# Kernel tuning notes

Hardware: AMD Instinct MI355X
Metric: run time of the kernel (lower is better)

## Reference

```python
import jax, jax.numpy as jnp
import numpy as np

D = 512
H = 8
HD = D // H
EPS = 1e-5
NEG_INF = -1e30


def _ln(x, g, b):
    mu = jnp.mean(x, axis=-1, keepdims=True)
    var = jnp.mean(jnp.square(x - mu), axis=-1, keepdims=True)
    return (x - mu) * jax.lax.rsqrt(var + EPS) * g + b


def setup_inputs() -> dict:
    key = jax.random.key(0)
    ks = jax.random.split(key, 8)
    V, M, S = 128, 128, 514  # seq includes 2 head tokens (cls+dist)
    inp = {
        "video_embeds": jax.random.normal(ks[0], (V, D), jnp.float32),
        "music_features": jax.random.normal(ks[1], (M, S, D), jnp.float32),
        "music_masks": jnp.ones((M, S - 2), jnp.int32),
    }
    wk = jax.random.split(ks[2], 5)
    for name, k in zip(["Wq", "Wk", "Wv", "Wo", "Wl"], wk):
        inp[name] = jax.random.normal(k, (D, D), jnp.float32) * 0.02
    for name in ["bq", "bk", "bv", "bo", "bl"]:
        inp[name] = jnp.zeros((D,), jnp.float32)
    for name in ["g1", "g2", "g3"]:
        inp[name] = jnp.ones((D,), jnp.float32)
    for name in ["b1", "b2", "b3"]:
        inp[name] = jnp.zeros((D,), jnp.float32)
    return inp


def reference(video_embeds, music_features, music_masks,
              Wq, bq, Wk, bk, Wv, bv, Wo, bo, Wl, bl,
              g1, b1, g2, b2, g3, b3):
    # drop cls + dist tokens
    mf = music_features[:, 2:, :]  # (M, f, D)
    ve = _ln(video_embeds, g1, b1)  # (V, D)
    mf = _ln(mf, g1, b1)
    V = ve.shape[0]
    M, f, _ = mf.shape

    q = (ve @ Wq.T + bq).reshape(V, H, HD).transpose(1, 0, 2)        # (H, V, hd)
    k = (mf @ Wk.T + bk).reshape(M, f, H, HD).transpose(0, 2, 1, 3)  # (M, H, f, hd)
    v = (mf @ Wv.T + bv).reshape(M, f, H, HD).transpose(0, 2, 1, 3)  # (M, H, f, hd)

    logits = jnp.einsum('hvd,mhfd->vmhf', q, k) / np.sqrt(HD).astype(np.float32)
    mask = music_masks[None, :, None, :]  # (1, M, 1, f)
    logits = jnp.where(mask == 0, NEG_INF, logits)
    w = jax.nn.softmax(logits, axis=-1)
    attn = jnp.einsum('vmhf,mhfd->vmhd', w, v).reshape(V, M, D)
    attn = attn @ Wo.T + bo

    attn = _ln(attn, g2, b2)
    out = attn + (attn @ Wl.T + bl)  # dropout = identity in eval
    return _ln(out, g3, b3)
```

## Files before the change

### kernel.cpp

```cpp
#include <hip/hip_runtime.h>
#include <hip/hip_bf16.h>

typedef unsigned int uint;
typedef unsigned short ushort;
typedef __bf16 bf16;
typedef bf16 bf16x8 __attribute__((ext_vector_type(8)));
typedef float f32x4 __attribute__((ext_vector_type(4)));
typedef ushort ushort4v __attribute__((ext_vector_type(4)));

__device__ __forceinline__ float bf2f(ushort u) {
  union { uint u; float f; } v; v.u = ((uint)u) << 16; return v.f;
}
__device__ __forceinline__ ushort f2bf(float f) {
  union { float f; uint u; } v; v.f = f;
  uint u = v.u;
  uint r = (u + 0x7fffu + ((u >> 16) & 1u)) >> 16;
  return (ushort)r;
}

__device__ __forceinline__ void gl2lds16(const void* g, void* l) {
  __builtin_amdgcn_global_load_lds(
      (const __attribute__((address_space(1))) void*)g,
      (__attribute__((address_space(3))) void*)l, 16, 0, 0);
}

__device__ __forceinline__ void ln_rows0(
    int nrows, int blk, int nblk, int tid,
    const float* __restrict__ srcA,
    const float* __restrict__ g, const float* __restrict__ b,
    ushort* __restrict__ dst)
{
  const int l = tid & 63;
  const int nw = nblk * 4;
  for (int row = blk * 4 + (tid >> 6); row < nrows; row += nw) {
    const float* s = srcA + (size_t)row * 512;
    float x[8];
    float4 a0 = *(const float4*)(s + l * 4);
    float4 a1 = *(const float4*)(s + 256 + l * 4);
    x[0] = a0.x; x[1] = a0.y; x[2] = a0.z; x[3] = a0.w;
    x[4] = a1.x; x[5] = a1.y; x[6] = a1.z; x[7] = a1.w;
    float sum = 0.f, sq = 0.f;
    #pragma unroll
    for (int j = 0; j < 8; ++j) { sum += x[j]; sq += x[j] * x[j]; }
    #pragma unroll
    for (int o = 1; o < 64; o <<= 1) {
      sum += __shfl_xor(sum, o);
      sq  += __shfl_xor(sq, o);
    }
    float mu = sum * (1.f / 512.f);
    float var = sq * (1.f / 512.f) - mu * mu;
    float rstd = rsqrtf(var + 1e-5f);
    float4 g0 = *(const float4*)(g + l * 4);
    float4 g1 = *(const float4*)(g + 256 + l * 4);
    float4 b0 = *(const float4*)(b + l * 4);
    float4 b1 = *(const float4*)(b + 256 + l * 4);
    float gv[8] = {g0.x,g0.y,g0.z,g0.w,g1.x,g1.y,g1.z,g1.w};
    float bv[8] = {b0.x,b0.y,b0.z,b0.w,b1.x,b1.y,b1.z,b1.w};
    ushort* d = dst + (size_t)row * 512;
    ushort4v p0, p1;
    #pragma unroll
    for (int j = 0; j < 4; ++j) {
      p0[j] = f2bf((x[j] - mu) * rstd * gv[j] + bv[j]);
      p1[j] = f2bf((x[4+j] - mu) * rstd * gv[4+j] + bv[4+j]);
    }
    *(ushort4v*)(d + l * 4) = p0;
    *(ushort4v*)(d + 256 + l * 4) = p1;
  }
}

__device__ __forceinline__ void ln_pair(
    int mode, int wid, int tid,
    const void* __restrict__ srcA, const void* __restrict__ srcB,
    const float* __restrict__ g, const float* __restrict__ b,
    void* __restrict__ dst)
{
  const int l = tid & 63;
  const int r0 = wid * 2, r1 = r0 + 1;
  float x0[8], x1[8];
  if (mode == 1) {
    int mm0 = r0 >> 9, fi0 = r0 & 511;
    int mm1 = r1 >> 9, fi1 = r1 & 511;
    const float* s0 = (const float*)srcA + ((size_t)mm0 * 514 + 2 + fi0) * 512;
    const float* s1 = (const float*)srcA + ((size_t)mm1 * 514 + 2 + fi1) * 512;
    float4 a0 = *(const float4*)(s0 + l * 4);
    float4 a1 = *(const float4*)(s0 + 256 + l * 4);
    float4 c0 = *(const float4*)(s1 + l * 4);
    float4 c1 = *(const float4*)(s1 + 256 + l * 4);
    x0[0]=a0.x; x0[1]=a0.y; x0[2]=a0.z; x0[3]=a0.w;
    x0[4]=a1.x; x0[5]=a1.y; x0[6]=a1.z; x0[7]=a1.w;
    x1[0]=c0.x; x1[1]=c0.y; x1[2]=c0.z; x1[3]=c0.w;
    x1[4]=c1.x; x1[5]=c1.y; x1[6]=c1.z; x1[7]=c1.w;
  } else if (mode == 2) {
    const ushort* s0 = (const ushort*)srcA + (size_t)r0 * 512;
    const ushort* s1 = (const ushort*)srcA + (size_t)r1 * 512;
    uint4 u0 = *(const uint4*)(s0 + l * 8);
    uint4 u1 = *(const uint4*)(s1 + l * 8);
    x0[0]=bf2f((ushort)u0.x); x0[1]=bf2f((ushort)(u0.x>>16));
    x0[2]=bf2f((ushort)u0.y); x0[3]=bf2f((ushort)(u0.y>>16));
    x0[4]=bf2f((ushort)u0.z); x0[5]=bf2f((ushort)(u0.z>>16));
    x0[6]=bf2f((ushort)u0.w); x0[7]=bf2f((ushort)(u0.w>>16));
    x1[0]=bf2f((ushort)u1.x); x1[1]=bf2f((ushort)(u1.x>>16));
    x1[2]=bf2f((ushort)u1.y); x1[3]=bf2f((ushort)(u1.y>>16));
    x1[4]=bf2f((ushort)u1.z); x1[5]=bf2f((ushort)(u1.z>>16));
    x1[6]=bf2f((ushort)u1.w); x1[7]=bf2f((ushort)(u1.w>>16));
  } else {
    const ushort* sa0 = (const ushort*)srcA + (size_t)r0 * 512;
    const ushort* sb0 = (const ushort*)srcB + (size_t)r0 * 512;
    const ushort* sa1 = (const ushort*)srcA + (size_t)r1 * 512;
    const ushort* sb1 = (const ushort*)srcB + (size_t)r1 * 512;
    uint4 ua0 = *(const uint4*)(sa0 + l * 8);
    uint4 ub0 = *(const uint4*)(sb0 + l * 8);
    uint4 ua1 = *(const uint4*)(sa1 + l * 8);
    uint4 ub1 = *(const uint4*)(sb1 + l * 8);
    x0[0]=bf2f((ushort)ua0.x)+bf2f((ushort)ub0.x);
    x0[1]=bf2f((ushort)(ua0.x>>16))+bf2f((ushort)(ub0.x>>16));
    x0[2]=bf2f((ushort)ua0.y)+bf2f((ushort)ub0.y);
    x0[3]=bf2f((ushort)(ua0.y>>16))+bf2f((ushort)(ub0.y>>16));
    x0[4]=bf2f((ushort)ua0.z)+bf2f((ushort)ub0.z);
    x0[5]=bf2f((ushort)(ua0.z>>16))+bf2f((ushort)(ub0.z>>16));
    x0[6]=bf2f((ushort)ua0.w)+bf2f((ushort)ub0.w);
    x0[7]=bf2f((ushort)(ua0.w>>16))+bf2f((ushort)(ub0.w>>16));
    x1[0]=bf2f((ushort)ua1.x)+bf2f((ushort)ub1.x);
    x1[1]=bf2f((ushort)(ua1.x>>16))+bf2f((ushort)(ub1.x>>16));
    x1[2]=bf2f((ushort)ua1.y)+bf2f((ushort)ub1.y);
    x1[3]=bf2f((ushort)(ua1.y>>16))+bf2f((ushort)(ub1.y>>16));
    x1[4]=bf2f((ushort)ua1.z)+bf2f((ushort)ub1.z);
    x1[5]=bf2f((ushort)(ua1.z>>16))+bf2f((ushort)(ub1.z>>16));
    x1[6]=bf2f((ushort)ua1.w)+bf2f((ushort)ub1.w);
    x1[7]=bf2f((ushort)(ua1.w>>16))+bf2f((ushort)(ub1.w>>16));
  }
  float s0 = 0.f, q0 = 0.f, s1 = 0.f, q1 = 0.f;
  #pragma unroll
  for (int j = 0; j < 8; ++j) {
    s0 += x0[j]; q0 += x0[j] * x0[j];
    s1 += x1[j]; q1 += x1[j] * x1[j];
  }
  #pragma unroll
  for (int o = 1; o < 64; o <<= 1) {
    s0 += __shfl_xor(s0, o); q0 += __shfl_xor(q0, o);
    s1 += __shfl_xor(s1, o); q1 += __shfl_xor(q1, o);
  }
  float mu0 = s0 * (1.f/512.f), mu1 = s1 * (1.f/512.f);
  float rstd0 = rsqrtf(q0 * (1.f/512.f) - mu0 * mu0 + 1e-5f);
  float rstd1 = rsqrtf(q1 * (1.f/512.f) - mu1 * mu1 + 1e-5f);

  float gv[8], bv[8];
  if (mode == 1) {
    float4 g0 = *(const float4*)(g + l * 4);
    float4 g1v = *(const float4*)(g + 256 + l * 4);
    float4 b0 = *(const float4*)(b + l * 4);
    float4 b1v = *(const float4*)(b + 256 + l * 4);
    gv[0]=g0.x; gv[1]=g0.y; gv[2]=g0.z; gv[3]=g0.w;
    gv[4]=g1v.x; gv[5]=g1v.y; gv[6]=g1v.z; gv[7]=g1v.w;
    bv[0]=b0.x; bv[1]=b0.y; bv[2]=b0.z; bv[3]=b0.w;
    bv[4]=b1v.x; bv[5]=b1v.y; bv[6]=b1v.z; bv[7]=b1v.w;
  } else {
    float4 g0 = *(const float4*)(g + l * 8);
    float4 g1v = *(const float4*)(g + l * 8 + 4);
    float4 b0 = *(const float4*)(b + l * 8);
    float4 b1v = *(const float4*)(b + l * 8 + 4);
    gv[0]=g0.x; gv[1]=g0.y; gv[2]=g0.z; gv[3]=g0.w;
    gv[4]=g1v.x; gv[5]=g1v.y; gv[6]=g1v.z; gv[7]=g1v.w;
    bv[0]=b0.x; bv[1]=b0.y; bv[2]=b0.z; bv[3]=b0.w;
    bv[4]=b1v.x; bv[5]=b1v.y; bv[6]=b1v.z; bv[7]=b1v.w;
  }
  if (mode == 1) {
    ushort* d0 = (ushort*)dst + (size_t)r0 * 512;
    ushort* d1 = (ushort*)dst + (size_t)r1 * 512;
    ushort4v p00, p01, p10, p11;
    #pragma unroll
    for (int j = 0; j < 4; ++j) {
      p00[j] = f2bf((x0[j]-mu0)*rstd0*gv[j]+bv[j]);
      p01[j] = f2bf((x0[4+j]-mu0)*rstd0*gv[4+j]+bv[4+j]);
      p10[j] = f2bf((x1[j]-mu1)*rstd1*gv[j]+bv[j]);
      p11[j] = f2bf((x1[4+j]-mu1)*rstd1*gv[4+j]+bv[4+j]);
    }
    *(ushort4v*)(d0 + l * 4) = p00;
    *(ushort4v*)(d0 + 256 + l * 4) = p01;
    *(ushort4v*)(d1 + l * 4) = p10;
    *(ushort4v*)(d1 + 256 + l * 4) = p11;
  } else if (mode == 2) {
    ushort* d0 = (ushort*)dst + (size_t)r0 * 512;
    ushort* d1 = (ushort*)dst + (size_t)r1 * 512;
    uint4 o0, o1;
    o0.x = (uint)f2bf((x0[0]-mu0)*rstd0*gv[0]+bv[0]) | ((uint)f2bf((x0[1]-mu0)*rstd0*gv[1]+bv[1]) << 16);
    o0.y = (uint)f2bf((x0[2]-mu0)*rstd0*gv[2]+bv[2]) | ((uint)f2bf((x0[3]-mu0)*rstd0*gv[3]+bv[3]) << 16);
    o0.z = (uint)f2bf((x0[4]-mu0)*rstd0*gv[4]+bv[4]) | ((uint)f2bf((x0[5]-mu0)*rstd0*gv[5]+bv[5]) << 16);
    o0.w = (uint)f2bf((x0[6]-mu0)*rstd0*gv[6]+bv[6]) | ((uint)f2bf((x0[7]-mu0)*rstd0*gv[7]+bv[7]) << 16);
    o1.x = (uint)f2bf((x1[0]-mu1)*rstd1*gv[0]+bv[0]) | ((uint)f2bf((x1[1]-mu1)*rstd1*gv[1]+bv[1]) << 16);
    o1.y = (uint)f2bf((x1[2]-mu1)*rstd1*gv[2]+bv[2]) | ((uint)f2bf((x1[3]-mu1)*rstd1*gv[3]+bv[3]) << 16);
    o1.z = (uint)f2bf((x1[4]-mu1)*rstd1*gv[4]+bv[4]) | ((uint)f2bf((x1[5]-mu1)*rstd1*gv[5]+bv[5]) << 16);
    o1.w = (uint)f2bf((x1[6]-mu1)*rstd1*gv[6]+bv[6]) | ((uint)f2bf((x1[7]-mu1)*rstd1*gv[7]+bv[7]) << 16);
    *(uint4*)(d0 + l * 8) = o0;
    *(uint4*)(d1 + l * 8) = o1;
  } else {
    float* d0 = (float*)dst + (size_t)r0 * 512;
    float* d1 = (float*)dst + (size_t)r1 * 512;
    float4 a0, a1, c0, c1;
    a0.x=(x0[0]-mu0)*rstd0*gv[0]+bv[0]; a0.y=(x0[1]-mu0)*rstd0*gv[1]+bv[1];
    a0.z=(x0[2]-mu0)*rstd0*gv[2]+bv[2]; a0.w=(x0[3]-mu0)*rstd0*gv[3]+bv[3];
    a1.x=(x0[4]-mu0)*rstd0*gv[4]+bv[4]; a1.y=(x0[5]-mu0)*rstd0*gv[5]+bv[5];
    a1.z=(x0[6]-mu0)*rstd0*gv[6]+bv[6]; a1.w=(x0[7]-mu0)*rstd0*gv[7]+bv[7];
    c0.x=(x1[0]-mu1)*rstd1*gv[0]+bv[0]; c0.y=(x1[1]-mu1)*rstd1*gv[1]+bv[1];
    c0.z=(x1[2]-mu1)*rstd1*gv[2]+bv[2]; c0.w=(x1[3]-mu1)*rstd1*gv[3]+bv[3];
    c1.x=(x1[4]-mu1)*rstd1*gv[4]+bv[4]; c1.y=(x1[5]-mu1)*rstd1*gv[5]+bv[5];
    c1.z=(x1[6]-mu1)*rstd1*gv[6]+bv[6]; c1.w=(x1[7]-mu1)*rstd1*gv[7]+bv[7];
    *(float4*)(d0 + l * 8) = a0;
    *(float4*)(d0 + l * 8 + 4) = a1;
    *(float4*)(d1 + l * 8) = c0;
    *(float4*)(d1 + l * 8 + 4) = c1;
  }
}

__global__ __launch_bounds__(256) void ln512p(
    int mode, const void* __restrict__ srcA, const void* __restrict__ srcB,
    const float* __restrict__ g, const float* __restrict__ b,
    void* __restrict__ dst)
{
  ln_pair(mode, blockIdx.x * 4 + (threadIdx.x >> 6), threadIdx.x, srcA, srcB, g, b, dst);
}

struct PreArgs {
  const float* s0; const float* s1; const float* s2; const float* s3; const float* s4;
  ushort* d0; ushort* d1; ushort* d2; ushort* d3; ushort* d4;
  const float* video; const float* music;
  const float* g1; const float* b1;
  ushort* veln; ushort* mfln;
};
__global__ __launch_bounds__(256) void preamble(PreArgs a) {
  int bb = blockIdx.x;
  if (bb < 640) {
    int t = bb * 256 + threadIdx.x;
    int which = t >> 15;
    int e = (t & 32767) * 8;
    const float* s = which == 0 ? a.s0 : which == 1 ? a.s1 : which == 2 ? a.s2 : which == 3 ? a.s3 : a.s4;
    ushort*      d = which == 0 ? a.d0 : which == 1 ? a.d1 : which == 2 ? a.d2 : which == 3 ? a.d3 : a.d4;
    float4 v0 = *(const float4*)(s + e);
    float4 v1 = *(const float4*)(s + e + 4);
    uint4 o;
    o.x = (uint)f2bf(v0.x) | ((uint)f2bf(v0.y) << 16);
    o.y = (uint)f2bf(v0.z) | ((uint)f2bf(v0.w) << 16);
    o.z = (uint)f2bf(v1.x) | ((uint)f2bf(v1.y) << 16);
    o.w = (uint)f2bf(v1.z) | ((uint)f2bf(v1.w) << 16);
    *(uint4*)(d + e) = o;
  } else if (bb < 672) {
    ln_rows0(128, bb - 640, 32, threadIdx.x, a.video, a.g1, a.b1, a.veln);
  } else {
    ln_pair(1, (bb - 672) * 4 + (threadIdx.x >> 6), threadIdx.x,
            a.music, nullptr, a.g1, a.b1, a.mfln);
  }
}

__global__ __launch_bounds__(512) void gemm_kvq(
    const ushort* __restrict__ Amf, const ushort* __restrict__ Aq,
    const ushort* __restrict__ Wk, const ushort* __restrict__ Wv,
    const ushort* __restrict__ Wq,
    const float* __restrict__ bk, const float* __restrict__ bv,
    const float* __restrict__ bq,
    ushort* __restrict__ K, ushort* __restrict__ Vt, ushort* __restrict__ Q)
{
  __shared__ __align__(16) ushort As[2][256 * 64];
  __shared__ __align__(16) ushort Bks[2][128 * 64];
  __shared__ __align__(16) ushort Bvs[2][128 * 64];
  const int tid = threadIdx.x;
  const int w = tid >> 6, l = tid & 63;
  const int lg = l >> 4, lr = l & 15;
  const int wr = w >> 1, wc = w & 1;

  const bool isq = (blockIdx.y == 256);
  const int row0 = isq ? 0 : blockIdx.y * 256;
  const int col0 = blockIdx.x * 128;
  const ushort* Ap  = isq ? Aq : Amf;
  const ushort* Wkp = isq ? Wq : Wk;

  f32x4 kacc[4][4], vacc[4][4];
  #pragma unroll
  for (int i = 0; i < 4; i++)
    #pragma unroll
    for (int j = 0; j < 4; j++) {
      f32x4 z = {0.f,0.f,0.f,0.f};
      kacc[i][j] = z; vacc[i][j] = z;
    }

  size_t asrc[4], wksrc[2], wvsrc[2]; int aldst[4], wldst[2];
  {
    int r = tid >> 3, j = tid & 7;
    int koff = (j ^ (r & 7)) * 8;
    #pragma unroll
    for (int c2 = 0; c2 < 4; ++c2) {
      asrc[c2] = (size_t)(row0 + c2 * 64 + r) * 512 + koff;
      aldst[c2] = ((c2 * 64 + w * 8) * 64);
    }
    #pragma unroll
    for (int c2 = 0; c2 < 2; ++c2) {
      wksrc[c2] = (size_t)(col0 + c2 * 64 + r) * 512 + koff;
      wvsrc[c2] = wksrc[c2];
      wldst[c2] = ((c2 * 64 + w * 8) * 64);
    }
  }

  auto stage = [&](int pb, int kk) {
    #pragma unroll
    for (int c2 = 0; c2 < 4; ++c2)
      gl2lds16(Ap + asrc[c2] + kk * 64, &As[pb][aldst[c2]]);
    #pragma unroll
    for (int c2 = 0; c2 < 2; ++c2) {
      gl2lds16(Wkp + wksrc[c2] + kk * 64, &Bks[pb][wldst[c2]]);
      gl2lds16(Wv + wvsrc[c2] + kk * 64, &Bvs[pb][wldst[c2]]);
    }
  };
  auto compute = [&](int pb) {
    #pragma unroll
    for (int ks = 0; ks < 2; ++ks) {
      bf16x8 af[4], bkf[4];
      #pragma unroll
      for (int mi = 0; mi < 4; ++mi) {
        int r = wr * 64 + mi * 16 + lr;
        af[mi] = *(const bf16x8*)(&As[pb][r * 64 + ((ks * 32 + lg * 8) ^ ((r & 7) * 8))]);
      }
      #pragma unroll
      for (int ni = 0; ni < 4; ++ni) {
        int r = wc * 64 + ni * 16 + lr;
        bkf[ni] = *(const bf16x8*)(&Bks[pb][r * 64 + ((ks * 32 + lg * 8) ^ ((r & 7) * 8))]);
      }
      #pragma unroll
      for (int mi = 0; mi < 4; ++mi)
        #pragma unroll
        for (int ni = 0; ni < 4; ++ni)
          kacc[mi][ni] = __builtin_amdgcn_mfma_f32_16x16x32_bf16(af[mi], bkf[ni], kacc[mi][ni], 0, 0, 0);
      if (!isq) {
        bf16x8 bvf[4];
        #pragma unroll
        for (int ni = 0; ni < 4; ++ni) {
          int r = wc * 64 + ni * 16 + lr;
          bvf[ni] = *(const bf16x8*)(&Bvs[pb][r * 64 + ((ks * 32 + lg * 8) ^ ((r & 7) * 8))]);
        }
        #pragma unroll
        for (int mi = 0; mi < 4; ++mi)
          #pragma unroll
          for (int ni = 0; ni < 4; ++ni)
            vacc[mi][ni] = __builtin_amdgcn_mfma_f32_16x16x32_bf16(af[mi], bvf[ni], vacc[mi][ni], 0, 0, 0);
      }
    }
  };

  stage(0, 0);
  __syncthreads();
  int cur = 0;
  #pragma unroll
  for (int kk = 0; kk < 7; ++kk) {
    stage(cur ^ 1, kk + 1);
    compute(cur);
    __syncthreads();
    cur ^= 1;
  }
  compute(cur);

  #pragma unroll
  for (int ni = 0; ni < 4; ++ni) {
    int cg = col0 + wc * 64 + ni * 16 + lr;
    float bkc = isq ? bq[cg] : bk[cg];
    float bvc = isq ? 0.f : bv[cg];
    #pragma unroll
    for (int mi = 0; mi < 4; ++mi) {
      int rg0 = row0 + wr * 64 + mi * 16 + lg * 4;
      if (isq) {
        if (rg0 < 128) {
          #pragma unroll
          for (int e = 0; e < 4; ++e)
            Q[(size_t)(rg0 + e) * 512 + cg] = f2bf((kacc[mi][ni][e] + bkc) * 0.125f);
        }
      } else {
        #pragma unroll
        for (int e = 0; e < 4; ++e)
          K[(size_t)(rg0 + e) * 512 + cg] = f2bf(kacc[mi][ni][e] + bkc);
        int m = rg0 >> 9, fi = rg0 & 511;
        ushort4v pk;
        #pragma unroll
        for (int e = 0; e < 4; ++e) pk[e] = f2bf(vacc[mi][ni][e] + bvc);
        *(ushort4v*)(Vt + (size_t)(m * 512 + cg) * 512 + fi) = pk;
      }
    }
  }
}

__global__ __launch_bounds__(512) void gemm_t3w(
    const ushort* __restrict__ A, const ushort* __restrict__ W,
    const float* __restrict__ bias, ushort* __restrict__ C,
    float scale, int vt_mode)
{
  __shared__ __align__(16) ushort As[2][256 * 64];
  __shared__ __align__(16) ushort Bs[2][128 * 64];
  const int tid = threadIdx.x;
  const int w = tid >> 6, l = tid & 63;
  const int lg = l >> 4, lr = l & 15;
  const int wr = w >> 1, wc = w & 1;

  int nwg = gridDim.x * gridDim.y;
  int bid = blockIdx.y * gridDim.x + blockIdx.x;
  if ((nwg & 7) == 0) bid = (bid & 7) * (nwg >> 3) + (bid >> 3);
  const int bx = bid % gridDim.x, by = bid / gridDim.x;
  const int row0 = by * 256, col0 = bx * 128;

  f32x4 acc[4][4];
  #pragma unroll
  for (int i = 0; i < 4; i++)
    #pragma unroll
    for (int j = 0; j < 4; j++) { f32x4 z = {0.f,0.f,0.f,0.f}; acc[i][j] = z; }

  size_t asrc[4], wsrc[2]; int aldst[4], wldst[2];
  {
    int r = tid >> 3, j = tid & 7;
    int koff = (j ^ (r & 7)) * 8;
    #pragma unroll
    for (int c2 = 0; c2 < 4; ++c2) {
      asrc[c2] = (size_t)(row0 + c2 * 64 + r) * 512 + koff;
      aldst[c2] = ((c2 * 64 + (w * 8)) * 64);
    }
    #pragma unroll
    for (int c2 = 0; c2 < 2; ++c2) {
      wsrc[c2] = (size_t)(col0 + c2 * 64 + r) * 512 + koff;
      wldst[c2] = ((c2 * 64 + (w * 8)) * 64);
    }
  }

  auto stage = [&](int pb, int kk) {
    #pragma unroll
    for (int c2 = 0; c2 < 4; ++c2)
      gl2lds16(A + asrc[c2] + kk * 64, &As[pb][aldst[c2]]);
    #pragma unroll
    for (int c2 = 0; c2 < 2; ++c2)
      gl2lds16(W + wsrc[c2] + kk * 64, &Bs[pb][wldst[c2]]);
  };
  auto compute = [&](int pb) {
    #pragma unroll
    for (int ks = 0; ks < 2; ++ks) {
      bf16x8 af[4], bfr[4];
      #pragma unroll
      for (int mi = 0; mi < 4; ++mi) {
        int r = wr * 64 + mi * 16 + lr;
        af[mi] = *(const bf16x8*)(&As[pb][r * 64 + ((ks * 32 + lg * 8) ^ ((r & 7) * 8))]);
      }
      #pragma unroll
      for (int ni = 0; ni < 4; ++ni) {
        int r = wc * 64 + ni * 16 + lr;
        bfr[ni] = *(const bf16x8*)(&Bs[pb][r * 64 + ((ks * 32 + lg * 8) ^ ((r & 7) * 8))]);
      }
      #pragma unroll
      for (int mi = 0; mi < 4; ++mi)
        #pragma unroll
        for (int ni = 0; ni < 4; ++ni)
          acc[mi][ni] = __builtin_amdgcn_mfma_f32_16x16x32_bf16(af[mi], bfr[ni], acc[mi][ni], 0, 0, 0);
    }
  };

  stage(0, 0);
  __syncthreads();
  int cur = 0;
  #pragma unroll
  for (int kk = 0; kk < 7; ++kk) {
    stage(cur ^ 1, kk + 1);
    compute(cur);
    __syncthreads();
    cur ^= 1;
  }
  compute(cur);

  #pragma unroll
  for (int ni = 0; ni < 4; ++ni) {
    int cg = col0 + wc * 64 + ni * 16 + lr;
    float bc = bias[cg];
    #pragma unroll
    for (int mi = 0; mi < 4; ++mi) {
      int rg0 = row0 + wr * 64 + mi * 16 + lg * 4;
      if (!vt_mode) {
        #pragma unroll
        for (int e = 0; e < 4; ++e) {
          float v = (acc[mi][ni][e] + bc) * scale;
          C[(size_t)(rg0 + e) * 512 + cg] = f2bf(v);
        }
      } else {
        int m = rg0 >> 9, fi = rg0 & 511;
        ushort4v pk;
        #pragma unroll
        for (int e = 0; e < 4; ++e) pk[e] = f2bf((acc[mi][ni][e] + bc) * scale);
        *(ushort4v*)(C + (size_t)(m * 512 + cg) * 512 + fi) = pk;
      }
    }
  }
}

__global__ __launch_bounds__(256) void attn_kernel(
    const ushort* __restrict__ q, const ushort* __restrict__ k,
    const ushort* __restrict__ vt, const int* __restrict__ masks,
    ushort* __restrict__ attn)
{
  __shared__ __align__(16) ushort Qs[128 * 64];
  __shared__ __align__(16) ushort Ks[2][64 * 64];
  __shared__ __align__(16) ushort Vs[2][64 * 64];
  __shared__ __align__(16) ushort Ps[4][32 * 64];
  __shared__ float maskf[2][64];
  __shared__ float stats[4][32];

  const int tid = threadIdx.x;
  const int w = tid >> 6, l = tid & 63;
  const int lg = l >> 4, lr = l & 15;
  const int m = blockIdx.x >> 3, h = blockIdx.x & 7;

  const size_t kbase = (size_t)(m * 512) * 512 + h * 64;
  const size_t vbase = (size_t)(m * 512 + h * 64) * 512;

  int sr = tid >> 2;
  auto stageKV = [&](int pb, int it) {
    const int f0 = it * 64;
    #pragma unroll
    for (int c2 = 0; c2 < 2; ++c2) {
      int c = c2 * 256 + tid;
      int r = c >> 3, j = c & 7;
      int off = (j * 8) ^ ((r & 7) * 8);
      gl2lds16(k + kbase + (size_t)(f0 + r) * 512 + off, &Ks[pb][(c2 * 256 + w * 64) * 8]);
      gl2lds16(vt + vbase + (size_t)r * 512 + f0 + off, &Vs[pb][(c2 * 256 + w * 64) * 8]);
    }
    if (tid < 64) maskf[pb][tid] = masks[m * 512 + f0 + tid] ? 0.f : -1e30f;
  };

  #pragma unroll
  for (int c2 = 0; c2 < 4; ++c2) {
    int c = c2 * 256 + tid;
    int r = c >> 3, j = c & 7;
    gl2lds16(q + (size_t)r * 512 + h * 64 + ((j * 8) ^ ((r & 7) * 8)),
             Qs + (c2 * 256 + w * 64) * 8);
  }
  stageKV(0, 0);
  __syncthreads();

  f32x4 acc[2][4];
  #pragma unroll
  for (int i = 0; i < 2; i++)
    #pragma unroll
    for (int j = 0; j < 4; j++) { f32x4 z = {0.f,0.f,0.f,0.f}; acc[i][j] = z; }
  float m_run[2] = {-INFINITY, -INFINITY};
  float l_run[2] = {0.f, 0.f};
  bf16x8 qf[2][2];
  #pragma unroll
  for (int nv = 0; nv < 2; ++nv)
    #pragma unroll
    for (int k2 = 0; k2 < 2; ++k2) {
      int v = w * 32 + nv * 16 + lr;
      qf[nv][k2] = *(const bf16x8*)(Qs + v * 64 + ((k2 * 32 + lg * 8) ^ ((v & 7) * 8)));
    }

  int cur = 0;
  for (int it = 0; it < 8; ++it) {
    if (it < 7) stageKV(cur ^ 1, it + 1);

    f32x4 s[4][2];
    #pragma unroll
    for (int mi = 0; mi < 4; mi++)
      #pragma unroll
      for (int nv = 0; nv < 2; nv++) { f32x4 z = {0.f,0.f,0.f,0.f}; s[mi][nv] = z; }
    #pragma unroll
    for (int k2 = 0; k2 < 2; ++k2) {
      bf16x8 kf[4];
      #pragma unroll
      for (int mi = 0; mi < 4; ++mi) {
        int f = mi * 16 + lr;
        kf[mi] = *(const bf16x8*)(&Ks[cur][f * 64 + ((k2 * 32 + lg * 8) ^ ((f & 7) * 8))]);
      }
      __builtin_amdgcn_s_setprio(1);
      #pragma unroll
      for (int mi = 0; mi < 4; ++mi)
        #pragma unroll
        for (int nv = 0; nv < 2; ++nv)
          s[mi][nv] = __builtin_amdgcn_mfma_f32_16x16x32_bf16(kf[mi], qf[nv][k2], s[mi][nv], 0, 0, 0);
      __builtin_amdgcn_s_setprio(0);
    }

    float mk[4][4];
    #pragma unroll
    for (int mi = 0; mi < 4; mi++)
      #pragma unroll
      for (int e = 0; e < 4; e++) mk[mi][e] = maskf[cur][mi * 16 + lg * 4 + e];

    #pragma unroll
    for (int nv = 0; nv < 2; ++nv) {
      float pmax = -INFINITY;
      #pragma unroll
      for (int mi = 0; mi < 4; mi++)
        #pragma unroll
        for (int e = 0; e < 4; e++) {
          s[mi][nv][e] += mk[mi][e];
          pmax = fmaxf(pmax, s[mi][nv][e]);
        }
      pmax = fmaxf(pmax, __shfl_xor(pmax, 16));
      pmax = fmaxf(pmax, __shfl_xor(pmax, 32));
      bool skip = __all(pmax - m_run[nv] <= 8.f);
      float mnew = skip ? m_run[nv] : fmaxf(m_run[nv], pmax);
      float sc = skip ? 1.f : __expf(m_run[nv] - mnew);
      float csum = 0.f;
      int vloc = nv * 16 + lr;
      #pragma unroll
      for (int mi = 0; mi < 4; mi++) {
        ushort4v pk;
        #pragma unroll
        for (int e = 0; e < 4; e++) {
          float p = __expf(s[mi][nv][e] - mnew);
          csum += p;
          pk[e] = f2bf(p);
        }
        int f = mi * 16 + lg * 4;
        *(ushort4v*)(&Ps[w][vloc * 64 + (f ^ ((vloc & 7) * 8))]) = pk;
      }
      csum += __shfl_xor(csum, 16);
      csum += __shfl_xor(csum, 32);
      l_run[nv] = l_run[nv] * sc + csum;
      m_run[nv] = mnew;
      if (lg == 0) stats[w][vloc] = sc;
      if (!skip) {
        int mi2 = nv;
        #pragma unroll
        for (int e = 0; e < 4; ++e) {
          float scv = stats[w][mi2 * 16 + lg * 4 + e];
          #pragma unroll
          for (int nd = 0; nd < 4; ++nd) acc[mi2][nd][e] *= scv;
        }
      }
    }

    #pragma unroll
    for (int k2 = 0; k2 < 2; ++k2) {
      bf16x8 pf[2], vf[4];
      #pragma unroll
      for (int mi2 = 0; mi2 < 2; ++mi2) {
        int vloc = mi2 * 16 + lr;
        pf[mi2] = *(const bf16x8*)(&Ps[w][vloc * 64 + ((k2 * 32 + lg * 8) ^ ((vloc & 7) * 8))]);
      }
      #pragma unroll
      for (int nd = 0; nd < 4; ++nd) {
        int d = nd * 16 + lr;
        vf[nd] = *(const bf16x8*)(&Vs[cur][d * 64 + ((k2 * 32 + lg * 8) ^ ((d & 7) * 8))]);
      }
      __builtin_amdgcn_s_setprio(1);
      #pragma unroll
      for (int mi2 = 0; mi2 < 2; ++mi2)
        #pragma unroll
        for (int nd = 0; nd < 4; ++nd)
          acc[mi2][nd] = __builtin_amdgcn_mfma_f32_16x16x32_bf16(pf[mi2], vf[nd], acc[mi2][nd], 0, 0, 0);
      __builtin_amdgcn_s_setprio(0);
    }
    __syncthreads();
    cur ^= 1;
  }

  #pragma unroll
  for (int nv = 0; nv < 2; ++nv)
    if (lg == 0) stats[w][nv * 16 + lr] = 1.f / l_run[nv];
  #pragma unroll
  for (int mi2 = 0; mi2 < 2; ++mi2)
    #pragma unroll
    for (int e = 0; e < 4; ++e) {
      float invl = stats[w][mi2 * 16 + lg * 4 + e];
      int vg = w * 32 + mi2 * 16 + lg * 4 + e;
      #pragma unroll
      for (int nd = 0; nd < 4; ++nd) {
        int d = nd * 16 + lr;
        attn[(size_t)(vg * 128 + m) * 512 + h * 64 + d] = f2bf(acc[mi2][nd][e] * invl);
      }
    }
}

extern "C" void kernel_launch(void* const* d_in, const int* in_sizes, int n_in,
                              void* d_out, int out_size, void* d_ws, size_t ws_size,
                              hipStream_t stream) {
  const float* video = (const float*)d_in[0];
  const float* music = (const float*)d_in[1];
  const int*   masks = (const int*)d_in[2];
  const float* Wq = (const float*)d_in[3];
  const float* Wk = (const float*)d_in[4];
  const float* Wv = (const float*)d_in[5];
  const float* Wo = (const float*)d_in[6];
  const float* Wl = (const float*)d_in[7];
  const float* bq = (const float*)d_in[8];
  const float* bk = (const float*)d_in[9];
  const float* bv = (const float*)d_in[10];
  const float* bo = (const float*)d_in[11];
  const float* bl = (const float*)d_in[12];
  const float* g1 = (const float*)d_in[13];
  const float* g2 = (const float*)d_in[14];
  const float* g3 = (const float*)d_in[15];
  const float* b1 = (const float*)d_in[16];
  const float* b2 = (const float*)d_in[17];
  const float* b3 = (const float*)d_in[18];

  char* ws = (char*)d_ws;
  ushort* mfln = (ushort*)(ws);
  ushort* kbuf = (ushort*)(ws + 67108864);
  ushort* vtb  = (ushort*)(ws + 134217728);
  ushort* attn = (ushort*)(ws + 201326592);
  ushort* c1   = (ushort*)(ws + 218103808);
  ushort* xbuf = (ushort*)(ws + 234881024);
  ushort* veln = (ushort*)(ws + 251658240);
  ushort* qbuf = (ushort*)(ws + 251789312);
  ushort* wqb  = (ushort*)(ws + 251920384);
  ushort* wkb  = wqb + 262144;
  ushort* wvb  = wkb + 262144;
  ushort* wob  = wvb + 262144;
  ushort* wlb  = wob + 262144;

  PreArgs pa = {Wq, Wk, Wv, Wo, Wl, wqb, wkb, wvb, wob, wlb,
                video, music, g1, b1, veln, mfln};
  preamble<<<8864, 256, 0, stream>>>(pa);

  gemm_kvq<<<dim3(4, 257), 512, 0, stream>>>(
      mfln, veln, wkb, wvb, wqb, bk, bv, bq, kbuf, vtb, qbuf);

  attn_kernel<<<1024, 256, 0, stream>>>(qbuf, kbuf, vtb, masks, attn);

  gemm_t3w<<<dim3(4, 64), 512, 0, stream>>>(attn, wob, bo, c1, 1.f, 0);
  ln512p<<<2048, 256, 0, stream>>>(2, c1, nullptr, g2, b2, xbuf);
  gemm_t3w<<<dim3(4, 64), 512, 0, stream>>>(xbuf, wlb, bl, c1, 1.f, 0);
  ln512p<<<2048, 256, 0, stream>>>(3, xbuf, c1, g3, b3, d_out);
}
```

Measured before the change: 271.7 us.

## Fuse output-projection GEMMs with bias, residual and LayerNorm epilogues

Replaces the two gemm_t3w + ln512p kernel pairs with a gemm_ln kernel. Each block computes 64 full rows across all 512 columns, so the LayerNorm can run in the epilogue using a cross-wave shared-memory reduction. This removes the bf16 intermediate round trips through c1 and two launches. The cost is fewer, larger blocks (256 blocks of 64 rows), a larger B tile in LDS, and uncoalesced scalar stores in the epilogue. It also adds s_setprio around the MFMA loop and trims the now-unused LN modes.

```diff
diff --git a/kernel.cpp b/kernel.cpp
--- a/kernel.cpp
+++ b/kernel.cpp
@@ -68,156 +68,61 @@
   }
 }
 
-__device__ __forceinline__ void ln_pair(
-    int mode, int wid, int tid,
-    const void* __restrict__ srcA, const void* __restrict__ srcB,
+__device__ __forceinline__ void ln_pair1(
+    int wid, int tid,
+    const float* __restrict__ srcA,
     const float* __restrict__ g, const float* __restrict__ b,
-    void* __restrict__ dst)
+    ushort* __restrict__ dst)
 {
   const int l = tid & 63;
   const int r0 = wid * 2, r1 = r0 + 1;
   float x0[8], x1[8];
-  if (mode == 1) {
-    int mm0 = r0 >> 9, fi0 = r0 & 511;
-    int mm1 = r1 >> 9, fi1 = r1 & 511;
-    const float* s0 = (const float*)srcA + ((size_t)mm0 * 514 + 2 + fi0) * 512;
-    const float* s1 = (const float*)srcA + ((size_t)mm1 * 514 + 2 + fi1) * 512;
-    float4 a0 = *(const float4*)(s0 + l * 4);
-    float4 a1 = *(const float4*)(s0 + 256 + l * 4);
-    float4 c0 = *(const float4*)(s1 + l * 4);
-    float4 c1 = *(const float4*)(s1 + 256 + l * 4);
-    x0[0]=a0.x; x0[1]=a0.y; x0[2]=a0.z; x0[3]=a0.w;
-    x0[4]=a1.x; x0[5]=a1.y; x0[6]=a1.z; x0[7]=a1.w;
-    x1[0]=c0.x; x1[1]=c0.y; x1[2]=c0.z; x1[3]=c0.w;
-    x1[4]=c1.x; x1[5]=c1.y; x1[6]=c1.z; x1[7]=c1.w;
-  } else if (mode == 2) {
-    const ushort* s0 = (const ushort*)srcA + (size_t)r0 * 512;
-    const ushort* s1 = (const ushort*)srcA + (size_t)r1 * 512;
-    uint4 u0 = *(const uint4*)(s0 + l * 8);
-    uint4 u1 = *(const uint4*)(s1 + l * 8);
-    x0[0]=bf2f((ushort)u0.x); x0[1]=bf2f((ushort)(u0.x>>16));
-    x0[2]=bf2f((ushort)u0.y); x0[3]=bf2f((ushort)(u0.y>>16));
-    x0[4]=bf2f((ushort)u0.z); x0[5]=bf2f((ushort)(u0.z>>16));
-    x0[6]=bf2f((ushort)u0.w); x0[7]=bf2f((ushort)(u0.w>>16));
-    x1[0]=bf2f((ushort)u1.x); x1[1]=bf2f((ushort)(u1.x>>16));
-    x1[2]=bf2f((ushort)u1.y); x1[3]=bf2f((ushort)(u1.y>>16));
-    x1[4]=bf2f((ushort)u1.z); x1[5]=bf2f((ushort)(u1.z>>16));
-    x1[6]=bf2f((ushort)u1.w); x1[7]=bf2f((ushort)(u1.w>>16));
-  } else {
-    const ushort* sa0 = (const ushort*)srcA + (size_t)r0 * 512;
-    const ushort* sb0 = (const ushort*)srcB + (size_t)r0 * 512;
-    const ushort* sa1 = (const ushort*)srcA + (size_t)r1 * 512;
-    const ushort* sb1 = (const ushort*)srcB + (size_t)r1 * 512;
-    uint4 ua0 = *(const uint4*)(sa0 + l * 8);
-    uint4 ub0 = *(const uint4*)(sb0 + l * 8);
-    uint4 ua1 = *(const uint4*)(sa1 + l * 8);
-    uint4 ub1 = *(const uint4*)(sb1 + l * 8);
-    x0[0]=bf2f((ushort)ua0.x)+bf2f((ushort)ub0.x);
-    x0[1]=bf2f((ushort)(ua0.x>>16))+bf2f((ushort)(ub0.x>>16));
-    x0[2]=bf2f((ushort)ua0.y)+bf2f((ushort)ub0.y);
-    x0[3]=bf2f((ushort)(ua0.y>>16))+bf2f((ushort)(ub0.y>>16));
-    x0[4]=bf2f((ushort)ua0.z)+bf2f((ushort)ub0.z);
-    x0[5]=bf2f((ushort)(ua0.z>>16))+bf2f((ushort)(ub0.z>>16));
-    x0[6]=bf2f((ushort)ua0.w)+bf2f((ushort)ub0.w);
-    x0[7]=bf2f((ushort)(ua0.w>>16))+bf2f((ushort)(ub0.w>>16));
-    x1[0]=bf2f((ushort)ua1.x)+bf2f((ushort)ub1.x);
-    x1[1]=bf2f((ushort)(ua1.x>>16))+bf2f((ushort)(ub1.x>>16));
-    x1[2]=bf2f((ushort)ua1.y)+bf2f((ushort)ub1.y);
-    x1[3]=bf2f((ushort)(ua1.y>>16))+bf2f((ushort)(ub1.y>>16));
-    x1[4]=bf2f((ushort)ua1.z)+bf2f((ushort)ub1.z);
-    x1[5]=bf2f((ushort)(ua1.z>>16))+bf2f((ushort)(ub1.z>>16));
-    x1[6]=bf2f((ushort)ua1.w)+bf2f((ushort)ub1.w);
-    x1[7]=bf2f((ushort)(ua1.w>>16))+bf2f((ushort)(ub1.w>>16));
-  }
-  float s0 = 0.f, q0 = 0.f, s1 = 0.f, q1 = 0.f;
+  int mm0 = r0 >> 9, fi0 = r0 & 511;
+  int mm1 = r1 >> 9, fi1 = r1 & 511;
+  const float* s0 = srcA + ((size_t)mm0 * 514 + 2 + fi0) * 512;
+  const float* s1 = srcA + ((size_t)mm1 * 514 + 2 + fi1) * 512;
+  float4 a0 = *(const float4*)(s0 + l * 4);
+  float4 a1 = *(const float4*)(s0 + 256 + l * 4);
+  float4 c0 = *(const float4*)(s1 + l * 4);
+  float4 c1 = *(const float4*)(s1 + 256 + l * 4);
+  x0[0]=a0.x; x0[1]=a0.y; x0[2]=a0.z; x0[3]=a0.w;
+  x0[4]=a1.x; x0[5]=a1.y; x0[6]=a1.z; x0[7]=a1.w;
+  x1[0]=c0.x; x1[1]=c0.y; x1[2]=c0.z; x1[3]=c0.w;
+  x1[4]=c1.x; x1[5]=c1.y; x1[6]=c1.z; x1[7]=c1.w;
+  float s0v = 0.f, q0 = 0.f, s1v = 0.f, q1 = 0.f;
   #pragma unroll
   for (int j = 0; j < 8; ++j) {
-    s0 += x0[j]; q0 += x0[j] * x0[j];
-    s1 += x1[j]; q1 += x1[j] * x1[j];
+    s0v += x0[j]; q0 += x0[j] * x0[j];
+    s1v += x1[j]; q1 += x1[j] * x1[j];
   }
   #pragma unroll
   for (int o = 1; o < 64; o <<= 1) {
-    s0 += __shfl_xor(s0, o); q0 += __shfl_xor(q0, o);
-    s1 += __shfl_xor(s1, o); q1 += __shfl_xor(q1, o);
-  }
-  float mu0 = s0 * (1.f/512.f), mu1 = s1 * (1.f/512.f);
+    s0v += __shfl_xor(s0v, o); q0 += __shfl_xor(q0, o);
+    s1v += __shfl_xor(s1v, o); q1 += __shfl_xor(q1, o);
+  }
+  float mu0 = s0v * (1.f/512.f), mu1 = s1v * (1.f/512.f);
   float rstd0 = rsqrtf(q0 * (1.f/512.f) - mu0 * mu0 + 1e-5f);
   float rstd1 = rsqrtf(q1 * (1.f/512.f) - mu1 * mu1 + 1e-5f);
-
-  float gv[8], bv[8];
-  if (mode == 1) {
-    float4 g0 = *(const float4*)(g + l * 4);
-    float4 g1v = *(const float4*)(g + 256 + l * 4);
-    float4 b0 = *(const float4*)(b + l * 4);
-    float4 b1v = *(const float4*)(b + 256 + l * 4);
-    gv[0]=g0.x; gv[1]=g0.y; gv[2]=g0.z; gv[3]=g0.w;
-    gv[4]=g1v.x; gv[5]=g1v.y; gv[6]=g1v.z; gv[7]=g1v.w;
-    bv[0]=b0.x; bv[1]=b0.y; bv[2]=b0.z; bv[3]=b0.w;
-    bv[4]=b1v.x; bv[5]=b1v.y; bv[6]=b1v.z; bv[7]=b1v.w;
-  } else {
-    float4 g0 = *(const float4*)(g + l * 8);
-    float4 g1v = *(const float4*)(g + l * 8 + 4);
-    float4 b0 = *(const float4*)(b + l * 8);
-    float4 b1v = *(const float4*)(b + l * 8 + 4);
-    gv[0]=g0.x; gv[1]=g0.y; gv[2]=g0.z; gv[3]=g0.w;
-    gv[4]=g1v.x; gv[5]=g1v.y; gv[6]=g1v.z; gv[7]=g1v.w;
-    bv[0]=b0.x; bv[1]=b0.y; bv[2]=b0.z; bv[3]=b0.w;
-    bv[4]=b1v.x; bv[5]=b1v.y; bv[6]=b1v.z; bv[7]=b1v.w;
-  }
-  if (mode == 1) {
-    ushort* d0 = (ushort*)dst + (size_t)r0 * 512;
-    ushort* d1 = (ushort*)dst + (size_t)r1 * 512;
-    ushort4v p00, p01, p10, p11;
-    #pragma unroll
-    for (int j = 0; j < 4; ++j) {
-      p00[j] = f2bf((x0[j]-mu0)*rstd0*gv[j]+bv[j]);
-      p01[j] = f2bf((x0[4+j]-mu0)*rstd0*gv[4+j]+bv[4+j]);
-      p10[j] = f2bf((x1[j]-mu1)*rstd1*gv[j]+bv[j]);
-      p11[j] = f2bf((x1[4+j]-mu1)*rstd1*gv[4+j]+bv[4+j]);
-    }
-    *(ushort4v*)(d0 + l * 4) = p00;
-    *(ushort4v*)(d0 + 256 + l * 4) = p01;
-    *(ushort4v*)(d1 + l * 4) = p10;
-    *(ushort4v*)(d1 + 256 + l * 4) = p11;
-  } else if (mode == 2) {
-    ushort* d0 = (ushort*)dst + (size_t)r0 * 512;
-    ushort* d1 = (ushort*)dst + (size_t)r1 * 512;
-    uint4 o0, o1;
-    o0.x = (uint)f2bf((x0[0]-mu0)*rstd0*gv[0]+bv[0]) | ((uint)f2bf((x0[1]-mu0)*rstd0*gv[1]+bv[1]) << 16);
-    o0.y = (uint)f2bf((x0[2]-mu0)*rstd0*gv[2]+bv[2]) | ((uint)f2bf((x0[3]-mu0)*rstd0*gv[3]+bv[3]) << 16);
-    o0.z = (uint)f2bf((x0[4]-mu0)*rstd0*gv[4]+bv[4]) | ((uint)f2bf((x0[5]-mu0)*rstd0*gv[5]+bv[5]) << 16);
-    o0.w = (uint)f2bf((x0[6]-mu0)*rstd0*gv[6]+bv[6]) | ((uint)f2bf((x0[7]-mu0)*rstd0*gv[7]+bv[7]) << 16);
-    o1.x = (uint)f2bf((x1[0]-mu1)*rstd1*gv[0]+bv[0]) | ((uint)f2bf((x1[1]-mu1)*rstd1*gv[1]+bv[1]) << 16);
-    o1.y = (uint)f2bf((x1[2]-mu1)*rstd1*gv[2]+bv[2]) | ((uint)f2bf((x1[3]-mu1)*rstd1*gv[3]+bv[3]) << 16);
-    o1.z = (uint)f2bf((x1[4]-mu1)*rstd1*gv[4]+bv[4]) | ((uint)f2bf((x1[5]-mu1)*rstd1*gv[5]+bv[5]) << 16);
-    o1.w = (uint)f2bf((x1[6]-mu1)*rstd1*gv[6]+bv[6]) | ((uint)f2bf((x1[7]-mu1)*rstd1*gv[7]+bv[7]) << 16);
-    *(uint4*)(d0 + l * 8) = o0;
-    *(uint4*)(d1 + l * 8) = o1;
-  } else {
-    float* d0 = (float*)dst + (size_t)r0 * 512;
-    float* d1 = (float*)dst + (size_t)r1 * 512;
-    float4 a0, a1, c0, c1;
-    a0.x=(x0[0]-mu0)*rstd0*gv[0]+bv[0]; a0.y=(x0[1]-mu0)*rstd0*gv[1]+bv[1];
-    a0.z=(x0[2]-mu0)*rstd0*gv[2]+bv[2]; a0.w=(x0[3]-mu0)*rstd0*gv[3]+bv[3];
-    a1.x=(x0[4]-mu0)*rstd0*gv[4]+bv[4]; a1.y=(x0[5]-mu0)*rstd0*gv[5]+bv[5];
-    a1.z=(x0[6]-mu0)*rstd0*gv[6]+bv[6]; a1.w=(x0[7]-mu0)*rstd0*gv[7]+bv[7];
-    c0.x=(x1[0]-mu1)*rstd1*gv[0]+bv[0]; c0.y=(x1[1]-mu1)*rstd1*gv[1]+bv[1];
-    c0.z=(x1[2]-mu1)*rstd1*gv[2]+bv[2]; c0.w=(x1[3]-mu1)*rstd1*gv[3]+bv[3];
-    c1.x=(x1[4]-mu1)*rstd1*gv[4]+bv[4]; c1.y=(x1[5]-mu1)*rstd1*gv[5]+bv[5];
-    c1.z=(x1[6]-mu1)*rstd1*gv[6]+bv[6]; c1.w=(x1[7]-mu1)*rstd1*gv[7]+bv[7];
-    *(float4*)(d0 + l * 8) = a0;
-    *(float4*)(d0 + l * 8 + 4) = a1;
-    *(float4*)(d1 + l * 8) = c0;
-    *(float4*)(d1 + l * 8 + 4) = c1;
-  }
-}
-
-__global__ __launch_bounds__(256) void ln512p(
-    int mode, const void* __restrict__ srcA, const void* __restrict__ srcB,
-    const float* __restrict__ g, const float* __restrict__ b,
-    void* __restrict__ dst)
-{
-  ln_pair(mode, blockIdx.x * 4 + (threadIdx.x >> 6), threadIdx.x, srcA, srcB, g, b, dst);
+  float4 g0 = *(const float4*)(g + l * 4);
+  float4 g1v = *(const float4*)(g + 256 + l * 4);
+  float4 b0 = *(const float4*)(b + l * 4);
+  float4 b1v = *(const float4*)(b + 256 + l * 4);
+  float gv[8] = {g0.x,g0.y,g0.z,g0.w,g1v.x,g1v.y,g1v.z,g1v.w};
+  float bv[8] = {b0.x,b0.y,b0.z,b0.w,b1v.x,b1v.y,b1v.z,b1v.w};
+  ushort* d0 = dst + (size_t)r0 * 512;
+  ushort* d1 = dst + (size_t)r1 * 512;
+  ushort4v p00, p01, p10, p11;
+  #pragma unroll
+  for (int j = 0; j < 4; ++j) {
+    p00[j] = f2bf((x0[j]-mu0)*rstd0*gv[j]+bv[j]);
+    p01[j] = f2bf((x0[4+j]-mu0)*rstd0*gv[4+j]+bv[4+j]);
+    p10[j] = f2bf((x1[j]-mu1)*rstd1*gv[j]+bv[j]);
+    p11[j] = f2bf((x1[4+j]-mu1)*rstd1*gv[4+j]+bv[4+j]);
+  }
+  *(ushort4v*)(d0 + l * 4) = p00;
+  *(ushort4v*)(d0 + 256 + l * 4) = p01;
+  *(ushort4v*)(d1 + l * 4) = p10;
+  *(ushort4v*)(d1 + 256 + l * 4) = p11;
 }
 
 struct PreArgs {
@@ -246,8 +151,8 @@
   } else if (bb < 672) {
     ln_rows0(128, bb - 640, 32, threadIdx.x, a.video, a.g1, a.b1, a.veln);
   } else {
-    ln_pair(1, (bb - 672) * 4 + (threadIdx.x >> 6), threadIdx.x,
-            a.music, nullptr, a.g1, a.b1, a.mfln);
+    ln_pair1((bb - 672) * 4 + (threadIdx.x >> 6), threadIdx.x,
+             a.music, a.g1, a.b1, a.mfln);
   }
 }
 
@@ -282,7 +187,7 @@
       kacc[i][j] = z; vacc[i][j] = z;
     }
 
-  size_t asrc[4], wksrc[2], wvsrc[2]; int aldst[4], wldst[2];
+  size_t asrc[4], wksrc[2]; int aldst[4], wldst[2];
   {
     int r = tid >> 3, j = tid & 7;
     int koff = (j ^ (r & 7)) * 8;
@@ -294,7 +199,6 @@
     #pragma unroll
     for (int c2 = 0; c2 < 2; ++c2) {
       wksrc[c2] = (size_t)(col0 + c2 * 64 + r) * 512 + koff;
-      wvsrc[c2] = wksrc[c2];
       wldst[c2] = ((c2 * 64 + w * 8) * 64);
     }
   }
@@ -306,7 +210,7 @@
     #pragma unroll
     for (int c2 = 0; c2 < 2; ++c2) {
       gl2lds16(Wkp + wksrc[c2] + kk * 64, &Bks[pb][wldst[c2]]);
-      gl2lds16(Wv + wvsrc[c2] + kk * 64, &Bvs[pb][wldst[c2]]);
+      gl2lds16(Wv + wksrc[c2] + kk * 64, &Bvs[pb][wldst[c2]]);
     }
   };
   auto compute = [&](int pb) {
@@ -384,23 +288,19 @@
   }
 }
 
-__global__ __launch_bounds__(512) void gemm_t3w(
+__global__ __launch_bounds__(512) void gemm_ln(
     const ushort* __restrict__ A, const ushort* __restrict__ W,
-    const float* __restrict__ bias, ushort* __restrict__ C,
-    float scale, int vt_mode)
+    const float* __restrict__ bias,
+    const float* __restrict__ gam, const float* __restrict__ bet,
+    void* __restrict__ outp, const ushort* __restrict__ resid, int outf32)
 {
-  __shared__ __align__(16) ushort As[2][256 * 64];
-  __shared__ __align__(16) ushort Bs[2][128 * 64];
+  __shared__ __align__(16) ushort As[2][64 * 64];
+  __shared__ __align__(16) ushort Bs[2][512 * 64];
+  __shared__ float red[8][64][2];
   const int tid = threadIdx.x;
   const int w = tid >> 6, l = tid & 63;
   const int lg = l >> 4, lr = l & 15;
-  const int wr = w >> 1, wc = w & 1;
-
-  int nwg = gridDim.x * gridDim.y;
-  int bid = blockIdx.y * gridDim.x + blockIdx.x;
-  if ((nwg & 7) == 0) bid = (bid & 7) * (nwg >> 3) + (bid >> 3);
-  const int bx = bid % gridDim.x, by = bid / gridDim.x;
-  const int row0 = by * 256, col0 = bx * 128;
+  const int row0 = blockIdx.x * 64;
 
   f32x4 acc[4][4];
   #pragma unroll
@@ -408,29 +308,21 @@
     #pragma unroll
     for (int j = 0; j < 4; j++) { f32x4 z = {0.f,0.f,0.f,0.f}; acc[i][j] = z; }
 
-  size_t asrc[4], wsrc[2]; int aldst[4], wldst[2];
+  size_t asrc, wsrc0; int aldst;
   {
     int r = tid >> 3, j = tid & 7;
     int koff = (j ^ (r & 7)) * 8;
-    #pragma unroll
-    for (int c2 = 0; c2 < 4; ++c2) {
-      asrc[c2] = (size_t)(row0 + c2 * 64 + r) * 512 + koff;
-      aldst[c2] = ((c2 * 64 + (w * 8)) * 64);
-    }
-    #pragma unroll
-    for (int c2 = 0; c2 < 2; ++c2) {
-      wsrc[c2] = (size_t)(col0 + c2 * 64 + r) * 512 + koff;
-      wldst[c2] = ((c2 * 64 + (w * 8)) * 64);
-    }
+    asrc = (size_t)(row0 + r) * 512 + koff;
+    wsrc0 = (size_t)r * 512 + koff;
+    aldst = (w * 8) * 64;
   }
 
   auto stage = [&](int pb, int kk) {
-    #pragma unroll
-    for (int c2 = 0; c2 < 4; ++c2)
-      gl2lds16(A + asrc[c2] + kk * 64, &As[pb][aldst[c2]]);
-    #pragma unroll
-    for (int c2 = 0; c2 < 2; ++c2)
-      gl2lds16(W + wsrc[c2] + kk * 64, &Bs[pb][wldst[c2]]);
+    gl2lds16(A + asrc + kk * 64, &As[pb][aldst]);
+    #pragma unroll
+    for (int b = 0; b < 8; ++b)
+      gl2lds16(W + wsrc0 + (size_t)b * 32768 + kk * 64,
+               &Bs[pb][(b * 64 + w * 8) * 64]);
   };
   auto compute = [&](int pb) {
     #pragma unroll
@@ -438,19 +330,21 @@
       bf16x8 af[4], bfr[4];
       #pragma unroll
       for (int mi = 0; mi < 4; ++mi) {
-        int r = wr * 64 + mi * 16 + lr;
-        af[mi] = *(const bf16x8*)(&As[pb][r * 64 + ((ks * 32 + lg * 8) ^ ((r & 7) * 8))]);
+        int ra = mi * 16 + lr;
+        af[mi] = *(const bf16x8*)(&As[pb][ra * 64 + ((ks * 32 + lg * 8) ^ ((ra & 7) * 8))]);
       }
       #pragma unroll
       for (int ni = 0; ni < 4; ++ni) {
-        int r = wc * 64 + ni * 16 + lr;
-        bfr[ni] = *(const bf16x8*)(&Bs[pb][r * 64 + ((ks * 32 + lg * 8) ^ ((r & 7) * 8))]);
-      }
+        int rb = w * 64 + ni * 16 + lr;
+        bfr[ni] = *(const bf16x8*)(&Bs[pb][rb * 64 + ((ks * 32 + lg * 8) ^ ((rb & 7) * 8))]);
+      }
+      __builtin_amdgcn_s_setprio(1);
       #pragma unroll
       for (int mi = 0; mi < 4; ++mi)
         #pragma unroll
         for (int ni = 0; ni < 4; ++ni)
           acc[mi][ni] = __builtin_amdgcn_mfma_f32_16x16x32_bf16(af[mi], bfr[ni], acc[mi][ni], 0, 0, 0);
+      __builtin_amdgcn_s_setprio(0);
     }
   };
 
@@ -466,28 +360,68 @@
   }
   compute(cur);
 
+  float bc[4], gv[4], bv2[4];
   #pragma unroll
   for (int ni = 0; ni < 4; ++ni) {
-    int cg = col0 + wc * 64 + ni * 16 + lr;
-    float bc = bias[cg];
-    #pragma unroll
-    for (int mi = 0; mi < 4; ++mi) {
-      int rg0 = row0 + wr * 64 + mi * 16 + lg * 4;
-      if (!vt_mode) {
-        #pragma unroll
-        for (int e = 0; e < 4; ++e) {
-          float v = (acc[mi][ni][e] + bc) * scale;
-          C[(size_t)(rg0 + e) * 512 + cg] = f2bf(v);
-        }
+    int col = w * 64 + ni * 16 + lr;
+    bc[ni] = bias[col];
+    gv[ni] = gam[col];
+    bv2[ni] = bet[col];
+  }
+  #pragma unroll
+  for (int mi = 0; mi < 4; ++mi)
+    #pragma unroll
+    for (int e = 0; e < 4; ++e) {
+      int row = row0 + mi * 16 + lg * 4 + e;
+      #pragma unroll
+      for (int ni = 0; ni < 4; ++ni) {
+        float v = acc[mi][ni][e] + bc[ni];
+        if (resid) v += bf2f(resid[(size_t)row * 512 + w * 64 + ni * 16 + lr]);
+        acc[mi][ni][e] = v;
+      }
+    }
+  #pragma unroll
+  for (int mi = 0; mi < 4; ++mi)
+    #pragma unroll
+    for (int e = 0; e < 4; ++e) {
+      float s = acc[mi][0][e] + acc[mi][1][e] + acc[mi][2][e] + acc[mi][3][e];
+      float q = acc[mi][0][e]*acc[mi][0][e] + acc[mi][1][e]*acc[mi][1][e]
+              + acc[mi][2][e]*acc[mi][2][e] + acc[mi][3][e]*acc[mi][3][e];
+      #pragma unroll
+      for (int o = 1; o < 16; o <<= 1) { s += __shfl_xor(s, o); q += __shfl_xor(q, o); }
+      if (lr == 0) {
+        int row = mi * 16 + lg * 4 + e;
+        red[w][row][0] = s;
+        red[w][row][1] = q;
+      }
+    }
+  __syncthreads();
+  #pragma unroll
+  for (int mi = 0; mi < 4; ++mi)
+    #pragma unroll
+    for (int e = 0; e < 4; ++e) {
+      int row = mi * 16 + lg * 4 + e;
+      float S = 0.f, Qm = 0.f;
+      #pragma unroll
+      for (int w2 = 0; w2 < 8; ++w2) { S += red[w2][row][0]; Qm += red[w2][row][1]; }
+      float mu = S * (1.f / 512.f);
+      float var = Qm * (1.f / 512.f) - mu * mu;
+      float rstd = rsqrtf(var + 1e-5f);
+      int grow = row0 + row;
+      if (!outf32) {
+        ushort* o = (ushort*)outp;
+        #pragma unroll
+        for (int ni = 0; ni < 4; ++ni)
+          o[(size_t)grow * 512 + w * 64 + ni * 16 + lr] =
+              f2bf((acc[mi][ni][e] - mu) * rstd * gv[ni] + bv2[ni]);
       } else {
-        int m = rg0 >> 9, fi = rg0 & 511;
-        ushort4v pk;
-        #pragma unroll
-        for (int e = 0; e < 4; ++e) pk[e] = f2bf((acc[mi][ni][e] + bc) * scale);
-        *(ushort4v*)(C + (size_t)(m * 512 + cg) * 512 + fi) = pk;
-      }
-    }
-  }
+        float* o = (float*)outp;
+        #pragma unroll
+        for (int ni = 0; ni < 4; ++ni)
+          o[(size_t)grow * 512 + w * 64 + ni * 16 + lr] =
+              (acc[mi][ni][e] - mu) * rstd * gv[ni] + bv2[ni];
+      }
+    }
 }
 
 __global__ __launch_bounds__(256) void attn_kernel(
@@ -510,7 +444,6 @@
   const size_t kbase = (size_t)(m * 512) * 512 + h * 64;
   const size_t vbase = (size_t)(m * 512 + h * 64) * 512;
 
-  int sr = tid >> 2;
   auto stageKV = [&](int pb, int it) {
     const int f0 = it * 64;
     #pragma unroll
@@ -697,7 +630,6 @@
   ushort* kbuf = (ushort*)(ws + 67108864);
   ushort* vtb  = (ushort*)(ws + 134217728);
   ushort* attn = (ushort*)(ws + 201326592);
-  ushort* c1   = (ushort*)(ws + 218103808);
   ushort* xbuf = (ushort*)(ws + 234881024);
   ushort* veln = (ushort*)(ws + 251658240);
   ushort* qbuf = (ushort*)(ws + 251789312);
@@ -716,8 +648,6 @@
 
   attn_kernel<<<1024, 256, 0, stream>>>(qbuf, kbuf, vtb, masks, attn);
 
-  gemm_t3w<<<dim3(4, 64), 512, 0, stream>>>(attn, wob, bo, c1, 1.f, 0);
-  ln512p<<<2048, 256, 0, stream>>>(2, c1, nullptr, g2, b2, xbuf);
-  gemm_t3w<<<dim3(4, 64), 512, 0, stream>>>(xbuf, wlb, bl, c1, 1.f, 0);
-  ln512p<<<2048, 256, 0, stream>>>(3, xbuf, c1, g3, b3, d_out);
-}
+  gemm_ln<<<256, 512, 0, stream>>>(attn, wob, bo, g2, b2, xbuf, nullptr, 0);
+  gemm_ln<<<256, 512, 0, stream>>>(xbuf, wlb, bl, g3, b3, d_out, xbuf, 1);
+}
```

After: 266.1 us (median of 3 runs). -2.0%, faster.
